# Kernel optimization log

Measured on AMD Instinct MI355X. Metric: run time of the kernel, lower is better.

The kernel has to match this reference:

```python
import jax, jax.numpy as jnp
import numpy as np

N_NODES = 10000
N_EDGES = 160000
N_FEAT = 512
HEADS = 8
HID = 128
OUT = 16


def setup_inputs() -> dict:
    key = jax.random.key(0)
    ks = jax.random.split(key, 16)
    inp = {
        'node_features': jax.random.normal(ks[0], (N_NODES, N_FEAT), jnp.float32),
        'edge_src': jax.random.randint(ks[1], (N_EDGES,), 0, N_NODES, jnp.int32),
        'edge_dst': jax.random.randint(ks[2], (N_EDGES,), 0, N_NODES, jnp.int32),
        # GAT layer params (scaled randn for numerical sanity)
        'W1': jax.random.normal(ks[3], (HEADS, HID, N_FEAT), jnp.float32) * 0.05,
        'a1': jax.random.normal(ks[4], (HEADS, 2 * HID), jnp.float32) * 0.05,
        'W2': jax.random.normal(ks[5], (HEADS, HID, HID), jnp.float32) * 0.05,
        'a2': jax.random.normal(ks[6], (HEADS, 2 * HID), jnp.float32) * 0.05,
        # MLP: LayerNorm(128) -> Linear(128,64) -> LeakyReLU -> Linear(64,16) -> LeakyReLU -> Linear(16,OUT) -> ReLU
        'ln_g': jnp.ones((HID,), jnp.float32),
        'ln_b': jnp.zeros((HID,), jnp.float32),
        'Wl1': jax.random.normal(ks[7], (64, HID), jnp.float32) * 0.05,
        'bl1': jnp.zeros((64,), jnp.float32),
        'Wl2': jax.random.normal(ks[8], (16, 64), jnp.float32) * 0.05,
        'bl2': jnp.zeros((16,), jnp.float32),
        'Wl3': jax.random.normal(ks[9], (OUT, 16), jnp.float32) * 0.05,
        'bl3': jnp.zeros((OUT,), jnp.float32),
    }
    return inp


def gat_layer(x, src, dst, W, a, n_nodes):
    # per-node, per-head projection: h[n,h,d]
    h = jnp.einsum('hdf,nf->nhd', W, x)
    # split attention vector: e_ij = a[:HID].h_i + a[HID:].h_j
    s_i = jnp.einsum('nhd,hd->nh', h, a[:, :HID])  # score contribution of target i
    s_j = jnp.einsum('nhd,hd->nh', h, a[:, HID:])  # score contribution of neighbor j
    e = jax.nn.leaky_relu(s_i[dst] + s_j[src])     # [E,H], negative_slope=0.01 (torch default)
    # segment softmax over edges grouped by dst
    m = jax.ops.segment_max(e, dst, num_segments=n_nodes)           # [N,H]
    m = jnp.where(jnp.isfinite(m), m, 0.0)
    ex = jnp.exp(e - m[dst])                                        # [E,H]
    denom = jax.ops.segment_sum(ex, dst, num_segments=n_nodes)      # [N,H]
    alpha = ex / jnp.where(denom > 0, denom, 1.0)[dst]              # [E,H]
    # scatter-accumulate weighted neighbor embeddings
    agg = jax.ops.segment_sum(alpha[:, :, None] * h[src], dst, num_segments=n_nodes)  # [N,H,HID]
    # average over heads, ELU (matches 1/attn_heads * attn_sum -> ELU)
    return jax.nn.elu(agg.mean(axis=1))  # [N,HID]


def reference(node_features, edge_src, edge_dst, W1, a1, W2, a2,
              ln_g, ln_b, Wl1, bl1, Wl2, bl2, Wl3, bl3):
    n = node_features.shape[0]
    emb1 = gat_layer(node_features, edge_src, edge_dst, W1, a1, n)
    emb2 = gat_layer(emb1, edge_src, edge_dst, W2, a2, n)
    g = emb2.mean(axis=0)  # [HID] graph embedding
    # MLP head (dropout = identity at inference)
    mu = g.mean()
    var = ((g - mu) ** 2).mean()
    gn = (g - mu) / jnp.sqrt(var + 1e-5) * ln_g + ln_b
    x = jax.nn.leaky_relu(Wl1 @ gn + bl1)
    x = jax.nn.leaky_relu(Wl2 @ x + bl2)
    return jax.nn.relu(Wl3 @ x + bl3)
```

## Files before the change

### kernel.cpp

```cpp
#include <hip/hip_runtime.h>
#include <math.h>

#define N_NODES 10000
#define N_EDGES 160000
#define N_FEAT  512
#define HEADS   8
#define HID     128

typedef __attribute__((ext_vector_type(8))) short bf16x8;
typedef __attribute__((ext_vector_type(4))) float f32x4;
typedef __attribute__((ext_vector_type(2))) float v2f;

__device__ inline unsigned short f2bf_rne(float f) {
  unsigned int u = __float_as_uint(f);
  unsigned int r = u + 0x7fffu + ((u >> 16) & 1u);
  return (unsigned short)(r >> 16);
}
__device__ inline float bf2f(unsigned int b) {
  return __uint_as_float(b << 16);
}

__device__ inline void split_body(const float* __restrict__ in,
                                  unsigned short* __restrict__ hi,
                                  unsigned short* __restrict__ lo,
                                  int R, int K8, int idx) {
  int r = idx & 15;
  int t = idx >> 4;
  int kq = t % K8;
  int rb = t / K8;
  int row = rb * 16 + r;
  float v[8] = {0.f, 0.f, 0.f, 0.f, 0.f, 0.f, 0.f, 0.f};
  if (row < R) {
    const float* p = in + (size_t)row * (K8 * 8) + kq * 8;
    float4 a = *(const float4*)p;
    float4 b = *(const float4*)(p + 4);
    v[0] = a.x; v[1] = a.y; v[2] = a.z; v[3] = a.w;
    v[4] = b.x; v[5] = b.y; v[6] = b.z; v[7] = b.w;
  }
  union { unsigned short u[8]; int4 v4; } H, L;
  #pragma unroll
  for (int e = 0; e < 8; ++e) {
    unsigned short hb_ = f2bf_rne(v[e]);
    H.u[e] = hb_;
    L.u[e] = f2bf_rne(v[e] - bf2f(hb_));
  }
  *(int4*)&hi[(size_t)idx * 8] = H.v4;
  if (lo) *(int4*)&lo[(size_t)idx * 8] = L.v4;
}

__global__ __launch_bounds__(256)
void split_frag2(const float* __restrict__ in1, unsigned short* __restrict__ hi1,
                 int R1, int K81, int total1, int nb1,
                 const float* __restrict__ in2, unsigned short* __restrict__ hi2,
                 int R2, int K82, int total2, int nb2,
                 const int* __restrict__ edst, int* __restrict__ deg, int E,
                 const float* __restrict__ av1, const float* __restrict__ W2p,
                 const float* __restrict__ av2,
                 float* __restrict__ wt1, float* __restrict__ wt2) {
  int b = (int)blockIdx.x;
  int tid = threadIdx.x;
  if (b < nb1) {
    int idx = b * 256 + tid;
    if (idx < total1) split_body(in1, hi1, nullptr, R1, K81, idx);
  } else if (b < nb1 + nb2) {
    int idx = (b - nb1) * 256 + tid;
    if (idx < total2) split_body(in2, hi2, nullptr, R2, K82, idx);
  } else {
    int nbE = (E + 255) / 256;
    int eb = b - nb1 - nb2;
    if (eb < nbE) {
      int e = eb * 256 + tid;
      if (e < E) atomicAdd(&deg[edst[e]], 1);
    } else {
      int wb = eb - nbE;
      if (wb < 32) {
        int o = wb * 256 + tid;
        int f = o & 511, ii = (o >> 9) & 1, h = o >> 10;
        const float* Wp = in2 + (size_t)h * HID * N_FEAT + f;
        const float* ap = av1 + h * 2 * HID + ii * HID;
        float c0 = 0.f, c1 = 0.f;
        for (int d = 0; d < HID; d += 2) {
          c0 = fmaf(Wp[(size_t)d * N_FEAT], ap[d], c0);
          c1 = fmaf(Wp[(size_t)(d + 1) * N_FEAT], ap[d + 1], c1);
        }
        wt1[o] = c0 + c1;
      } else {
        int o = (wb - 32) * 256 + tid;
        int f = o & 127, ii = (o >> 7) & 1, h = o >> 8;
        const float* Wp = W2p + (size_t)h * HID * HID + f;
        const float* ap = av2 + h * 2 * HID + ii * HID;
        float c0 = 0.f, c1 = 0.f;
        for (int d = 0; d < HID; d += 2) {
          c0 = fmaf(Wp[(size_t)d * HID], ap[d], c0);
          c1 = fmaf(Wp[(size_t)(d + 1) * HID], ap[d + 1], c1);
        }
        wt2[o] = c0 + c1;
      }
    }
  }
}

__global__ __launch_bounds__(256, 3)
void gemm_frag(const unsigned short* __restrict__ Afh,
               const unsigned short* __restrict__ Bfh,
               unsigned short* __restrict__ hb,
               int M, int K) {
  int tid = threadIdx.x;
  int wave = tid >> 6, lane = tid & 63;
  int r = lane & 15, q = lane >> 4;
  int wr = wave >> 1, wc = wave & 1;

  int blk = blockIdx.x;
  int mtile = blk % 80;
  int head = blk / 80;
  int m0 = mtile * 128;
  int K8 = K >> 3;

  const bf16x8* pA = (const bf16x8*)Afh;
  const bf16x8* pB = (const bf16x8*)Bfh;
  size_t rstep = (size_t)K8 * 16;
  size_t aidx = (size_t)((m0 >> 4) + wr * 4) * rstep + (size_t)q * 16 + r;
  size_t bidx = (size_t)(head * 8 + wc * 4) * rstep + (size_t)q * 16 + r;

  f32x4 acc[4][4] = {};

  for (int k0 = 0; k0 < K; k0 += 64, aidx += 128, bidx += 128) {
    bf16x8 a[8], b[8];
    #pragma unroll
    for (int i = 0; i < 4; ++i) {
      a[i]     = pA[aidx + i * rstep];
      b[i]     = pB[bidx + i * rstep];
      a[i + 4] = pA[aidx + i * rstep + 64];
      b[i + 4] = pB[bidx + i * rstep + 64];
    }
    #pragma unroll
    for (int i = 0; i < 4; ++i)
      #pragma unroll
      for (int j = 0; j < 4; ++j)
        acc[i][j] = __builtin_amdgcn_mfma_f32_16x16x32_bf16(a[i], b[j], acc[i][j], 0, 0, 0);
    #pragma unroll
    for (int i = 0; i < 4; ++i)
      #pragma unroll
      for (int j = 0; j < 4; ++j)
        acc[i][j] = __builtin_amdgcn_mfma_f32_16x16x32_bf16(a[i + 4], b[j + 4], acc[i][j], 0, 0, 0);
  }

  #pragma unroll
  for (int i = 0; i < 4; ++i)
    #pragma unroll
    for (int reg = 0; reg < 4; ++reg) {
      int row = m0 + wr * 64 + i * 16 + q * 4 + reg;
      if (row < M) {
        #pragma unroll
        for (int j = 0; j < 4; ++j)
          hb[((size_t)head * M + row) * HID + wc * 64 + j * 16 + r] =
              f2bf_rne(acc[i][j][reg]);
      }
    }
}

__global__ __launch_bounds__(1024)
void scan_score(const int* __restrict__ deg, int* __restrict__ off, int N,
                const float* __restrict__ x, const float* __restrict__ wt1,
                float* __restrict__ si, float* __restrict__ sj) {
  if (blockIdx.x == 0) {
    __shared__ int sums[1024];
    const int PER = 10;
    int tid = threadIdx.x;
    int base = tid * PER;
    int loc[PER];
    int run = 0;
    #pragma unroll
    for (int j = 0; j < PER; ++j) {
      int v = (base + j < N) ? deg[base + j] : 0;
      run += v;
      loc[j] = run;
    }
    sums[tid] = run;
    __syncthreads();
    for (int o = 1; o < 1024; o <<= 1) {
      int v = (tid >= o) ? sums[tid - o] : 0;
      __syncthreads();
      sums[tid] += v;
      __syncthreads();
    }
    int ex = sums[tid] - run;
    if (tid == 0) off[0] = 0;
    #pragma unroll
    for (int j = 0; j < PER; ++j)
      if (base + j < N) off[base + j + 1] = ex + loc[j];
    return;
  }
  __shared__ float wl[8192];
  int tid = threadIdx.x;
  #pragma unroll
  for (int k = 0; k < 8; ++k) wl[tid + k * 1024] = wt1[tid + k * 1024];
  __syncthreads();
  int wv = tid >> 6, lane = tid & 63;
  int rr = lane >> 4, sl = lane & 15;
  int n = ((int)blockIdx.x - 1) * 64 + wv * 4 + rr;
  if (n >= N) return;
  const float* xp = x + (size_t)n * N_FEAT + sl * 4;
  float acc[16];
  #pragma unroll
  for (int t = 0; t < 16; ++t) acc[t] = 0.f;
  #pragma unroll
  for (int k = 0; k < 8; ++k) {
    float4 xv = *(const float4*)(xp + k * 64);
    #pragma unroll
    for (int t = 0; t < 16; ++t) {
      float4 w4 = *(const float4*)&wl[t * 512 + k * 64 + sl * 4];
      acc[t] = fmaf(xv.x, w4.x, fmaf(xv.y, w4.y, fmaf(xv.z, w4.z, fmaf(xv.w, w4.w, acc[t]))));
    }
  }
  #pragma unroll
  for (int o = 1; o <= 8; o <<= 1)
    #pragma unroll
    for (int t = 0; t < 16; ++t) acc[t] += __shfl_xor(acc[t], o);
  float out = acc[0];
  #pragma unroll
  for (int t = 1; t < 16; ++t) out = (sl == t) ? acc[t] : out;
  int h = sl >> 1;
  if (sl & 1) sj[(size_t)h * N + n] = out;
  else        si[(size_t)h * N + n] = out;
}

__global__ void fill_kernel(const int* __restrict__ src, const int* __restrict__ dst,
                            const int* __restrict__ off, int* __restrict__ cursor,
                            int* __restrict__ ssrc, int E) {
  int e = blockIdx.x * blockDim.x + threadIdx.x;
  if (e < E) {
    int d = dst[e];
    int p = atomicAdd(&cursor[d], 1);
    ssrc[off[d] + p] = src[e];
  }
}

__global__ __launch_bounds__(512)
void gat_aggregate8(const unsigned short* __restrict__ hb,
                    const float* __restrict__ si, const float* __restrict__ sj,
                    const int* __restrict__ off, const int* __restrict__ ssrc,
                    unsigned short* __restrict__ aggb, int N) {
  __shared__ int2 prs[8][4][32];
  int head = blockIdx.x & 7;
  int wv = threadIdx.x >> 6;
  int lane = threadIdx.x & 63;
  int grp = lane >> 4;
  int sl = lane & 15;
  int n = (blockIdx.x >> 3) * 32 + wv * 4 + grp;
  const unsigned short* hbase = hb + (size_t)head * N * HID;
  const float* sjh = sj + (size_t)head * N;
  bool nv = n < N;
  int begin = 0, deg = 0;
  float s_i = 0.f;
  if (nv) {
    begin = off[n];
    deg = off[n + 1] - begin;
    s_i = si[(size_t)head * N + n];
  }

  int src0 = 0, src1 = 0;
  float sc0 = -INFINITY, sc1 = -INFINITY;
  if (sl < deg) {
    src0 = ssrc[begin + sl];
    float t = s_i + sjh[src0];
    sc0 = t > 0.f ? t : 0.01f * t;
  }
  if (16 + sl < deg) {
    src1 = ssrc[begin + 16 + sl];
    float t = s_i + sjh[src1];
    sc1 = t > 0.f ? t : 0.01f * t;
  }
  float m = fmaxf(sc0, sc1);
  for (int e2 = 32 + sl; e2 < deg; e2 += 16) {
    int s = ssrc[begin + e2];
    float t = s_i + sjh[s];
    t = t > 0.f ? t : 0.01f * t;
    m = fmaxf(m, t);
  }
  #pragma unroll
  for (int o = 1; o <= 8; o <<= 1) m = fmaxf(m, __shfl_xor(m, o));

  float w0 = (sl < deg) ? __expf(sc0 - m) : 0.f;
  float w1 = (16 + sl < deg) ? __expf(sc1 - m) : 0.f;
  float den = w0 + w1;
  for (int e2 = 32 + sl; e2 < deg; e2 += 16) {
    int s = ssrc[begin + e2];
    float t = s_i + sjh[s];
    t = t > 0.f ? t : 0.01f * t;
    den += __expf(t - m);
  }
  #pragma unroll
  for (int o = 1; o <= 8; o <<= 1) den += __shfl_xor(den, o);

  prs[wv][grp][sl] = make_int2(src0, __float_as_int(w0));
  prs[wv][grp][16 + sl] = make_int2(src1, __float_as_int(w1));
  __asm__ volatile("s_waitcnt lgkmcnt(0)" ::: "memory");

  v2f a01 = {0.f, 0.f}, a23 = {0.f, 0.f}, a45 = {0.f, 0.f}, a67 = {0.f, 0.f};
  int dmin = deg < 32 ? deg : 32;
  for (int e0 = 0; e0 < dmin; e0 += 4) {
    int2 p[4];
    #pragma unroll
    for (int u = 0; u < 4; ++u) p[u] = prs[wv][grp][e0 + u];
    int4 pv[4];
    #pragma unroll
    for (int u = 0; u < 4; ++u)
      pv[u] = *(const int4*)&hbase[(size_t)p[u].x * HID + sl * 8];
    #pragma unroll
    for (int u = 0; u < 4; ++u) {
      float w = __int_as_float(p[u].y);
      v2f w2 = {w, w};
      int4 q = pv[u];
      v2f t0 = {bf2f((unsigned)q.x & 0xffffu), __uint_as_float((unsigned)q.x & 0xffff0000u)};
      v2f t1 = {bf2f((unsigned)q.y & 0xffffu), __uint_as_float((unsigned)q.y & 0xffff0000u)};
      v2f t2 = {bf2f((unsigned)q.z & 0xffffu), __uint_as_float((unsigned)q.z & 0xffff0000u)};
      v2f t3 = {bf2f((unsigned)q.w & 0xffffu), __uint_as_float((unsigned)q.w & 0xffff0000u)};
      a01 += w2 * t0;
      a23 += w2 * t1;
      a45 += w2 * t2;
      a67 += w2 * t3;
    }
  }
  for (int e2 = 32; e2 < deg; ++e2) {
    int s = ssrc[begin + e2];
    float t = s_i + sjh[s];
    t = t > 0.f ? t : 0.01f * t;
    float w = __expf(t - m);
    v2f w2 = {w, w};
    int4 q = *(const int4*)&hbase[(size_t)s * HID + sl * 8];
    v2f t0 = {bf2f((unsigned)q.x & 0xffffu), __uint_as_float((unsigned)q.x & 0xffff0000u)};
    v2f t1 = {bf2f((unsigned)q.y & 0xffffu), __uint_as_float((unsigned)q.y & 0xffff0000u)};
    v2f t2 = {bf2f((unsigned)q.z & 0xffffu), __uint_as_float((unsigned)q.z & 0xffff0000u)};
    v2f t3 = {bf2f((unsigned)q.w & 0xffffu), __uint_as_float((unsigned)q.w & 0xffff0000u)};
    a01 += w2 * t0; a23 += w2 * t1; a45 += w2 * t2; a67 += w2 * t3;
  }

  if (nv) {
    float inv = den > 0.f ? 1.0f / den : 0.f;
    union { unsigned short u[8]; int4 v4; } P;
    P.u[0] = f2bf_rne(a01.x * inv); P.u[1] = f2bf_rne(a01.y * inv);
    P.u[2] = f2bf_rne(a23.x * inv); P.u[3] = f2bf_rne(a23.y * inv);
    P.u[4] = f2bf_rne(a45.x * inv); P.u[5] = f2bf_rne(a45.y * inv);
    P.u[6] = f2bf_rne(a67.x * inv); P.u[7] = f2bf_rne(a67.y * inv);
    *(int4*)&aggb[((size_t)head * N + n) * HID + sl * 8] = P.v4;
  }
}

__global__ __launch_bounds__(256)
void headmean_frag_w2(const unsigned short* __restrict__ aggb,
                      unsigned short* __restrict__ hiA,
                      int N, int nbHM,
                      const float* __restrict__ W2, unsigned short* __restrict__ hiB,
                      int totalB,
                      const float* __restrict__ wt2,
                      float* __restrict__ si, float* __restrict__ sj) {
  if ((int)blockIdx.x >= nbHM) {
    int idx = (blockIdx.x - nbHM) * 256 + threadIdx.x;
    if (idx < totalB) split_body(W2, hiB, nullptr, HEADS * HID, 16, idx);
    return;
  }
  __shared__ float wl[2048];
  __shared__ float sred[16][16][17];
  int tid = threadIdx.x;
  #pragma unroll
  for (int k = 0; k < 8; ++k) wl[tid + k * 256] = wt2[tid + k * 256];
  __syncthreads();
  int idx = blockIdx.x * 256 + tid;
  int r = idx & 15;
  int kq = (idx >> 4) & 15;
  int rb = idx >> 8;
  int n = rb * 16 + r;
  float s[8] = {0.f, 0.f, 0.f, 0.f, 0.f, 0.f, 0.f, 0.f};
  if (n < N) {
    #pragma unroll
    for (int hh = 0; hh < HEADS; ++hh) {
      int4 pv = *(const int4*)&aggb[((size_t)hh * N + n) * HID + kq * 8];
      s[0] += bf2f((unsigned)pv.x & 0xffffu);
      s[1] += __uint_as_float((unsigned)pv.x & 0xffff0000u);
      s[2] += bf2f((unsigned)pv.y & 0xffffu);
      s[3] += __uint_as_float((unsigned)pv.y & 0xffff0000u);
      s[4] += bf2f((unsigned)pv.z & 0xffffu);
      s[5] += __uint_as_float((unsigned)pv.z & 0xffff0000u);
      s[6] += bf2f((unsigned)pv.w & 0xffffu);
      s[7] += __uint_as_float((unsigned)pv.w & 0xffff0000u);
    }
  }
  float p[16];
  #pragma unroll
  for (int t = 0; t < 16; ++t) p[t] = 0.f;
  union { unsigned short u[8]; int4 v4; } H;
  #pragma unroll
  for (int e = 0; e < 8; ++e) {
    float v = s[e] * (1.0f / HEADS);
    v = v > 0.f ? v : (__expf(v) - 1.0f);
    #pragma unroll
    for (int t = 0; t < 16; ++t) p[t] = fmaf(v, wl[t * 128 + kq * 8 + e], p[t]);
    H.u[e] = f2bf_rne(v);
  }
  *(int4*)&hiA[(size_t)idx * 8] = H.v4;
  #pragma unroll
  for (int t = 0; t < 16; ++t) sred[kq][r][t] = p[t];
  __syncthreads();
  {
    int rr = tid >> 4, t = tid & 15;
    float sum = 0.f;
    #pragma unroll
    for (int k = 0; k < 16; ++k) sum += sred[k][rr][t];
    int nn = rb * 16 + rr;
    if (nn < N) {
      int h = t >> 1;
      if (t & 1) sj[(size_t)h * N + nn] = sum;
      else       si[(size_t)h * N + nn] = sum;
    }
  }
}

__global__ __launch_bounds__(256)
void headmean_pool(const unsigned short* __restrict__ aggb, float* __restrict__ g,
                   int N) {
  __shared__ float sm[16][128];
  int t = threadIdx.x;
  int nl = t >> 4, dg = t & 15;
  int n = blockIdx.x * 16 + nl;
  float v[8] = {0.f, 0.f, 0.f, 0.f, 0.f, 0.f, 0.f, 0.f};
  if (n < N) {
    #pragma unroll
    for (int hh = 0; hh < HEADS; ++hh) {
      int4 pv = *(const int4*)&aggb[((size_t)hh * N + n) * HID + dg * 8];
      v[0] += bf2f((unsigned)pv.x & 0xffffu);
      v[1] += __uint_as_float((unsigned)pv.x & 0xffff0000u);
      v[2] += bf2f((unsigned)pv.y & 0xffffu);
      v[3] += __uint_as_float((unsigned)pv.y & 0xffff0000u);
      v[4] += bf2f((unsigned)pv.z & 0xffffu);
      v[5] += __uint_as_float((unsigned)pv.z & 0xffff0000u);
      v[6] += bf2f((unsigned)pv.w & 0xffffu);
      v[7] += __uint_as_float((unsigned)pv.w & 0xffff0000u);
    }
    #pragma unroll
    for (int e = 0; e < 8; ++e) {
      float x = v[e] * (1.0f / HEADS);
      v[e] = x > 0.f ? x : (__expf(x) - 1.0f);
    }
  }
  #pragma unroll
  for (int e = 0; e < 8; ++e) sm[nl][dg * 8 + e] = v[e];
  __syncthreads();
  if (t < 128) {
    float s = 0.f;
    #pragma unroll
    for (int nn = 0; nn < 16; ++nn) s += sm[nn][t];
    atomicAdd(&g[t], s);
  }
}

__global__ __launch_bounds__(128)
void mlp_kernel(const float* __restrict__ g, const float* __restrict__ ln_g,
                const float* __restrict__ ln_b, const float* __restrict__ Wl1,
                const float* __restrict__ bl1, const float* __restrict__ Wl2,
                const float* __restrict__ bl2, const float* __restrict__ Wl3,
                const float* __restrict__ bl3, float* __restrict__ out, float invN) {
  __shared__ float red[128];
  __shared__ float gn[128];
  __shared__ float x1[64];
  __shared__ float x2[16];
  int t = threadIdx.x;
  float gg = g[t] * invN;
  red[t] = gg;
  __syncthreads();
  for (int o = 64; o > 0; o >>= 1) {
    if (t < o) red[t] += red[t + o];
    __syncthreads();
  }
  float mu = red[0] * (1.0f / HID);
  __syncthreads();
  float dv = gg - mu;
  red[t] = dv * dv;
  __syncthreads();
  for (int o = 64; o > 0; o >>= 1) {
    if (t < o) red[t] += red[t + o];
    __syncthreads();
  }
  float var = red[0] * (1.0f / HID);
  gn[t] = dv / sqrtf(var + 1e-5f) * ln_g[t] + ln_b[t];
  __syncthreads();
  if (t < 64) {
    float s = bl1[t];
    for (int k = 0; k < 128; ++k) s += Wl1[t * 128 + k] * gn[k];
    x1[t] = s > 0.f ? s : 0.01f * s;
  }
  __syncthreads();
  if (t < 16) {
    float s = bl2[t];
    for (int k = 0; k < 64; ++k) s += Wl2[t * 64 + k] * x1[k];
    x2[t] = s > 0.f ? s : 0.01f * s;
  }
  __syncthreads();
  if (t < 16) {
    float s = bl3[t];
    for (int k = 0; k < 16; ++k) s += Wl3[t * 16 + k] * x2[k];
    out[t] = s > 0.f ? s : 0.f;
  }
}

extern "C" void kernel_launch(void* const* d_in, const int* in_sizes, int n_in,
                              void* d_out, int out_size, void* d_ws, size_t ws_size,
                              hipStream_t stream) {
  const float* x    = (const float*)d_in[0];
  const int*   esrc = (const int*)d_in[1];
  const int*   edst = (const int*)d_in[2];
  const float* W1   = (const float*)d_in[3];
  const float* a1   = (const float*)d_in[4];
  const float* W2   = (const float*)d_in[5];
  const float* a2   = (const float*)d_in[6];
  const float* ln_g = (const float*)d_in[7];
  const float* ln_b = (const float*)d_in[8];
  const float* Wl1  = (const float*)d_in[9];
  const float* bl1  = (const float*)d_in[10];
  const float* Wl2  = (const float*)d_in[11];
  const float* bl2  = (const float*)d_in[12];
  const float* Wl3  = (const float*)d_in[13];
  const float* bl3  = (const float*)d_in[14];
  float* out = (float*)d_out;

  const int RBPAD = 640;

  unsigned short* aggb = (unsigned short*)d_ws;
  float* si   = (float*)(aggb + (size_t)N_NODES * HEADS * HID);
  float* sj   = si + N_NODES * HEADS;
  float* g    = sj + N_NODES * HEADS;
  int*   deg  = (int*)(g + 128);
  int*   cur  = deg + N_NODES;
  int*   off  = cur + N_NODES;
  int*   ssrc = off + 10004;
  unsigned short* Afh = (unsigned short*)(ssrc + N_EDGES);
  float* wt1 = (float*)(Afh + (size_t)RBPAD * 64 * 128);
  float* wt2 = wt1 + 8192;
  unsigned short* Bfh = (unsigned short*)(wt1 + (size_t)RBPAD * 64 * 64);
  unsigned short* hb  = Bfh + (size_t)2 * 64 * 64 * 128;

  hipMemsetAsync(g, 0, 128 * sizeof(float) + 2 * N_NODES * sizeof(int), stream);

  int gemmGrid = 80 * HEADS;
  int aggGrid = ((N_NODES + 31) / 32) * 8;

  {
    int totalA = RBPAD * 64 * 16;
    int nbA = (totalA + 255) / 256;
    int totalB = 64 * 64 * 16;
    int nbB = (totalB + 255) / 256;
    int nbE = (N_EDGES + 255) / 256;
    int nbW = 40;
    split_frag2<<<nbA + nbB + nbE + nbW, 256, 0, stream>>>(
        x, Afh, N_NODES, 64, totalA, nbA,
        W1, Bfh, HEADS * HID, 64, totalB, nbB,
        edst, deg, N_EDGES,
        a1, W2, a2, wt1, wt2);
  }
  scan_score<<<1 + (N_NODES + 63) / 64, 1024, 0, stream>>>(deg, off, N_NODES,
                                                           x, wt1, si, sj);
  fill_kernel<<<(N_EDGES + 255) / 256, 256, 0, stream>>>(esrc, edst, off, cur, ssrc, N_EDGES);

  gemm_frag<<<gemmGrid, 256, 0, stream>>>(Afh, Bfh, hb, N_NODES, N_FEAT);
  gat_aggregate8<<<aggGrid, 512, 0, stream>>>(hb, si, sj, off, ssrc, aggb, N_NODES);
  {
    int nbHM = (N_NODES + 15) / 16;
    int totalB = 64 * 16 * 16;
    int nbB = (totalB + 255) / 256;
    headmean_frag_w2<<<nbHM + nbB, 256, 0, stream>>>(aggb, Afh, N_NODES, nbHM,
                                                     W2, Bfh, totalB,
                                                     wt2, si, sj);
  }

  gemm_frag<<<gemmGrid, 256, 0, stream>>>(Afh, Bfh, hb, N_NODES, HID);
  gat_aggregate8<<<aggGrid, 512, 0, stream>>>(hb, si, sj, off, ssrc, aggb, N_NODES);

  headmean_pool<<<(N_NODES + 15) / 16, 256, 0, stream>>>(aggb, g, N_NODES);
  mlp_kernel<<<1, 128, 0, stream>>>(g, ln_g, ln_b, Wl1, bl1, Wl2, bl2, Wl3, bl3,
                                    out, 1.0f / N_NODES);
}
```

Before: 251.7 us.

## Replace CSR build with fixed-slot adjacency and fuse score into GEMM launch

Replaces the degree count, prefix-scan and fill passes with a single pass that atomically places each edge's source into a fixed 32-slot bucket per destination, spilling extras to a global overflow list. This removes two kernel launches and their serialization. The layer-1 score computation is merged into the GEMM launch as extra blocks, and the W2 bf16 conversion moves into the first kernel. The aggregation loop is unrolled to 8 edges. Nodes with more than 32 in-edges now scan the whole overflow list, which is costly if such nodes are common. The order of edges within a node now depends on atomics, so floating-point summation order is nondeterministic.

```diff
diff --git a/kernel.cpp b/kernel.cpp
--- a/kernel.cpp
+++ b/kernel.cpp
@@ -22,7 +22,6 @@
 
 __device__ inline void split_body(const float* __restrict__ in,
                                   unsigned short* __restrict__ hi,
-                                  unsigned short* __restrict__ lo,
                                   int R, int K8, int idx) {
   int r = idx & 15;
   int t = idx >> 4;
@@ -37,15 +36,10 @@
     v[0] = a.x; v[1] = a.y; v[2] = a.z; v[3] = a.w;
     v[4] = b.x; v[5] = b.y; v[6] = b.z; v[7] = b.w;
   }
-  union { unsigned short u[8]; int4 v4; } H, L;
-  #pragma unroll
-  for (int e = 0; e < 8; ++e) {
-    unsigned short hb_ = f2bf_rne(v[e]);
-    H.u[e] = hb_;
-    L.u[e] = f2bf_rne(v[e] - bf2f(hb_));
-  }
+  union { unsigned short u[8]; int4 v4; } H;
+  #pragma unroll
+  for (int e = 0; e < 8; ++e) H.u[e] = f2bf_rne(v[e]);
   *(int4*)&hi[(size_t)idx * 8] = H.v4;
-  if (lo) *(int4*)&lo[(size_t)idx * 8] = L.v4;
 }
 
 __global__ __launch_bounds__(256)
@@ -53,24 +47,39 @@
                  int R1, int K81, int total1, int nb1,
                  const float* __restrict__ in2, unsigned short* __restrict__ hi2,
                  int R2, int K82, int total2, int nb2,
-                 const int* __restrict__ edst, int* __restrict__ deg, int E,
-                 const float* __restrict__ av1, const float* __restrict__ W2p,
-                 const float* __restrict__ av2,
+                 const float* __restrict__ W2p, unsigned short* __restrict__ hi3,
+                 int total3, int nb3,
+                 const int* __restrict__ esrc, const int* __restrict__ edst,
+                 int* __restrict__ deg, int* __restrict__ slots,
+                 int2* __restrict__ ovf, int* __restrict__ cnt, int E,
+                 const float* __restrict__ av1, const float* __restrict__ av2,
                  float* __restrict__ wt1, float* __restrict__ wt2) {
   int b = (int)blockIdx.x;
   int tid = threadIdx.x;
   if (b < nb1) {
     int idx = b * 256 + tid;
-    if (idx < total1) split_body(in1, hi1, nullptr, R1, K81, idx);
+    if (idx < total1) split_body(in1, hi1, R1, K81, idx);
   } else if (b < nb1 + nb2) {
     int idx = (b - nb1) * 256 + tid;
-    if (idx < total2) split_body(in2, hi2, nullptr, R2, K82, idx);
+    if (idx < total2) split_body(in2, hi2, R2, K82, idx);
+  } else if (b < nb1 + nb2 + nb3) {
+    int idx = (b - nb1 - nb2) * 256 + tid;
+    if (idx < total3) split_body(W2p, hi3, HEADS * HID, 16, idx);
   } else {
     int nbE = (E + 255) / 256;
-    int eb = b - nb1 - nb2;
+    int eb = b - nb1 - nb2 - nb3;
     if (eb < nbE) {
       int e = eb * 256 + tid;
-      if (e < E) atomicAdd(&deg[edst[e]], 1);
+      if (e < E) {
+        int d = edst[e], s = esrc[e];
+        int p = atomicAdd(&deg[d], 1);
+        if (p < 32) {
+          slots[d * 32 + p] = s;
+        } else {
+          int q = atomicAdd(&cnt[1], 1);
+          if (q < E) ovf[q] = make_int2(d, s);
+        }
+      }
     } else {
       int wb = eb - nbE;
       if (wb < 32) {
@@ -101,11 +110,48 @@
 }
 
 __global__ __launch_bounds__(256, 3)
-void gemm_frag(const unsigned short* __restrict__ Afh,
-               const unsigned short* __restrict__ Bfh,
-               unsigned short* __restrict__ hb,
-               int M, int K) {
+void gemm_score(const unsigned short* __restrict__ Afh,
+                const unsigned short* __restrict__ Bfh,
+                unsigned short* __restrict__ hb,
+                int M, int K, int nbGemm,
+                const float* __restrict__ x, const float* __restrict__ wt1,
+                float* __restrict__ si, float* __restrict__ sj, int N) {
   int tid = threadIdx.x;
+  if ((int)blockIdx.x >= nbGemm) {
+    __shared__ float wl[8192];
+    #pragma unroll
+    for (int k = 0; k < 32; ++k) wl[tid + k * 256] = wt1[tid + k * 256];
+    __syncthreads();
+    int wv = tid >> 6, lane = tid & 63;
+    int rr = lane >> 4, sl = lane & 15;
+    int n = ((int)blockIdx.x - nbGemm) * 16 + wv * 4 + rr;
+    if (n >= N) return;
+    const float* xp = x + (size_t)n * N_FEAT + sl * 4;
+    float acc[16];
+    #pragma unroll
+    for (int t = 0; t < 16; ++t) acc[t] = 0.f;
+    #pragma unroll
+    for (int k = 0; k < 8; ++k) {
+      float4 xv = *(const float4*)(xp + k * 64);
+      #pragma unroll
+      for (int t = 0; t < 16; ++t) {
+        float4 w4 = *(const float4*)&wl[t * 512 + k * 64 + sl * 4];
+        acc[t] = fmaf(xv.x, w4.x, fmaf(xv.y, w4.y, fmaf(xv.z, w4.z, fmaf(xv.w, w4.w, acc[t]))));
+      }
+    }
+    #pragma unroll
+    for (int o = 1; o <= 8; o <<= 1)
+      #pragma unroll
+      for (int t = 0; t < 16; ++t) acc[t] += __shfl_xor(acc[t], o);
+    float outv = acc[0];
+    #pragma unroll
+    for (int t = 1; t < 16; ++t) outv = (sl == t) ? acc[t] : outv;
+    int h = sl >> 1;
+    if (sl & 1) sj[(size_t)h * N + n] = outv;
+    else        si[(size_t)h * N + n] = outv;
+    return;
+  }
+
   int wave = tid >> 6, lane = tid & 63;
   int r = lane & 15, q = lane >> 4;
   int wr = wave >> 1, wc = wave & 1;
@@ -159,87 +205,11 @@
     }
 }
 
-__global__ __launch_bounds__(1024)
-void scan_score(const int* __restrict__ deg, int* __restrict__ off, int N,
-                const float* __restrict__ x, const float* __restrict__ wt1,
-                float* __restrict__ si, float* __restrict__ sj) {
-  if (blockIdx.x == 0) {
-    __shared__ int sums[1024];
-    const int PER = 10;
-    int tid = threadIdx.x;
-    int base = tid * PER;
-    int loc[PER];
-    int run = 0;
-    #pragma unroll
-    for (int j = 0; j < PER; ++j) {
-      int v = (base + j < N) ? deg[base + j] : 0;
-      run += v;
-      loc[j] = run;
-    }
-    sums[tid] = run;
-    __syncthreads();
-    for (int o = 1; o < 1024; o <<= 1) {
-      int v = (tid >= o) ? sums[tid - o] : 0;
-      __syncthreads();
-      sums[tid] += v;
-      __syncthreads();
-    }
-    int ex = sums[tid] - run;
-    if (tid == 0) off[0] = 0;
-    #pragma unroll
-    for (int j = 0; j < PER; ++j)
-      if (base + j < N) off[base + j + 1] = ex + loc[j];
-    return;
-  }
-  __shared__ float wl[8192];
-  int tid = threadIdx.x;
-  #pragma unroll
-  for (int k = 0; k < 8; ++k) wl[tid + k * 1024] = wt1[tid + k * 1024];
-  __syncthreads();
-  int wv = tid >> 6, lane = tid & 63;
-  int rr = lane >> 4, sl = lane & 15;
-  int n = ((int)blockIdx.x - 1) * 64 + wv * 4 + rr;
-  if (n >= N) return;
-  const float* xp = x + (size_t)n * N_FEAT + sl * 4;
-  float acc[16];
-  #pragma unroll
-  for (int t = 0; t < 16; ++t) acc[t] = 0.f;
-  #pragma unroll
-  for (int k = 0; k < 8; ++k) {
-    float4 xv = *(const float4*)(xp + k * 64);
-    #pragma unroll
-    for (int t = 0; t < 16; ++t) {
-      float4 w4 = *(const float4*)&wl[t * 512 + k * 64 + sl * 4];
-      acc[t] = fmaf(xv.x, w4.x, fmaf(xv.y, w4.y, fmaf(xv.z, w4.z, fmaf(xv.w, w4.w, acc[t]))));
-    }
-  }
-  #pragma unroll
-  for (int o = 1; o <= 8; o <<= 1)
-    #pragma unroll
-    for (int t = 0; t < 16; ++t) acc[t] += __shfl_xor(acc[t], o);
-  float out = acc[0];
-  #pragma unroll
-  for (int t = 1; t < 16; ++t) out = (sl == t) ? acc[t] : out;
-  int h = sl >> 1;
-  if (sl & 1) sj[(size_t)h * N + n] = out;
-  else        si[(size_t)h * N + n] = out;
-}
-
-__global__ void fill_kernel(const int* __restrict__ src, const int* __restrict__ dst,
-                            const int* __restrict__ off, int* __restrict__ cursor,
-                            int* __restrict__ ssrc, int E) {
-  int e = blockIdx.x * blockDim.x + threadIdx.x;
-  if (e < E) {
-    int d = dst[e];
-    int p = atomicAdd(&cursor[d], 1);
-    ssrc[off[d] + p] = src[e];
-  }
-}
-
 __global__ __launch_bounds__(512)
-void gat_aggregate8(const unsigned short* __restrict__ hb,
+void gat_aggregate9(const unsigned short* __restrict__ hb,
                     const float* __restrict__ si, const float* __restrict__ sj,
-                    const int* __restrict__ off, const int* __restrict__ ssrc,
+                    const int* __restrict__ deg, const int* __restrict__ slots,
+                    const int2* __restrict__ ovf, const int* __restrict__ cnt,
                     unsigned short* __restrict__ aggb, int N) {
   __shared__ int2 prs[8][4][32];
   int head = blockIdx.x & 7;
@@ -251,44 +221,55 @@
   const unsigned short* hbase = hb + (size_t)head * N * HID;
   const float* sjh = sj + (size_t)head * N;
   bool nv = n < N;
-  int begin = 0, deg = 0;
+  int dg = 0;
   float s_i = 0.f;
   if (nv) {
-    begin = off[n];
-    deg = off[n + 1] - begin;
+    dg = deg[n];
     s_i = si[(size_t)head * N + n];
   }
+  int sbase = n * 32;
 
   int src0 = 0, src1 = 0;
   float sc0 = -INFINITY, sc1 = -INFINITY;
-  if (sl < deg) {
-    src0 = ssrc[begin + sl];
+  if (sl < dg) {
+    src0 = slots[sbase + sl];
     float t = s_i + sjh[src0];
     sc0 = t > 0.f ? t : 0.01f * t;
   }
-  if (16 + sl < deg) {
-    src1 = ssrc[begin + 16 + sl];
+  if (16 + sl < dg) {
+    src1 = slots[sbase + 16 + sl];
     float t = s_i + sjh[src1];
     sc1 = t > 0.f ? t : 0.01f * t;
   }
   float m = fmaxf(sc0, sc1);
-  for (int e2 = 32 + sl; e2 < deg; e2 += 16) {
-    int s = ssrc[begin + e2];
-    float t = s_i + sjh[s];
-    t = t > 0.f ? t : 0.01f * t;
-    m = fmaxf(m, t);
+  int oc = 0;
+  if (dg > 32) {
+    oc = cnt[1];
+    if (oc > N_EDGES) oc = N_EDGES;
+    for (int e2 = sl; e2 < oc; e2 += 16) {
+      int2 pe = ovf[e2];
+      if (pe.x == n) {
+        float t = s_i + sjh[pe.y];
+        t = t > 0.f ? t : 0.01f * t;
+        m = fmaxf(m, t);
+      }
+    }
   }
   #pragma unroll
   for (int o = 1; o <= 8; o <<= 1) m = fmaxf(m, __shfl_xor(m, o));
 
-  float w0 = (sl < deg) ? __expf(sc0 - m) : 0.f;
-  float w1 = (16 + sl < deg) ? __expf(sc1 - m) : 0.f;
+  float w0 = (sl < dg) ? __expf(sc0 - m) : 0.f;
+  float w1 = (16 + sl < dg) ? __expf(sc1 - m) : 0.f;
   float den = w0 + w1;
-  for (int e2 = 32 + sl; e2 < deg; e2 += 16) {
-    int s = ssrc[begin + e2];
-    float t = s_i + sjh[s];
-    t = t > 0.f ? t : 0.01f * t;
-    den += __expf(t - m);
+  if (dg > 32) {
+    for (int e2 = sl; e2 < oc; e2 += 16) {
+      int2 pe = ovf[e2];
+      if (pe.x == n) {
+        float t = s_i + sjh[pe.y];
+        t = t > 0.f ? t : 0.01f * t;
+        den += __expf(t - m);
+      }
+    }
   }
   #pragma unroll
   for (int o = 1; o <= 8; o <<= 1) den += __shfl_xor(den, o);
@@ -298,17 +279,17 @@
   __asm__ volatile("s_waitcnt lgkmcnt(0)" ::: "memory");
 
   v2f a01 = {0.f, 0.f}, a23 = {0.f, 0.f}, a45 = {0.f, 0.f}, a67 = {0.f, 0.f};
-  int dmin = deg < 32 ? deg : 32;
-  for (int e0 = 0; e0 < dmin; e0 += 4) {
-    int2 p[4];
-    #pragma unroll
-    for (int u = 0; u < 4; ++u) p[u] = prs[wv][grp][e0 + u];
-    int4 pv[4];
-    #pragma unroll
-    for (int u = 0; u < 4; ++u)
+  int dmin = dg < 32 ? dg : 32;
+  for (int e0 = 0; e0 < dmin; e0 += 8) {
+    int2 p[8];
+    #pragma unroll
+    for (int u = 0; u < 8; ++u) p[u] = prs[wv][grp][e0 + u];
+    int4 pv[8];
+    #pragma unroll
+    for (int u = 0; u < 8; ++u)
       pv[u] = *(const int4*)&hbase[(size_t)p[u].x * HID + sl * 8];
     #pragma unroll
-    for (int u = 0; u < 4; ++u) {
+    for (int u = 0; u < 8; ++u) {
       float w = __int_as_float(p[u].y);
       v2f w2 = {w, w};
       int4 q = pv[u];
@@ -322,18 +303,21 @@
       a67 += w2 * t3;
     }
   }
-  for (int e2 = 32; e2 < deg; ++e2) {
-    int s = ssrc[begin + e2];
-    float t = s_i + sjh[s];
-    t = t > 0.f ? t : 0.01f * t;
-    float w = __expf(t - m);
-    v2f w2 = {w, w};
-    int4 q = *(const int4*)&hbase[(size_t)s * HID + sl * 8];
-    v2f t0 = {bf2f((unsigned)q.x & 0xffffu), __uint_as_float((unsigned)q.x & 0xffff0000u)};
-    v2f t1 = {bf2f((unsigned)q.y & 0xffffu), __uint_as_float((unsigned)q.y & 0xffff0000u)};
-    v2f t2 = {bf2f((unsigned)q.z & 0xffffu), __uint_as_float((unsigned)q.z & 0xffff0000u)};
-    v2f t3 = {bf2f((unsigned)q.w & 0xffffu), __uint_as_float((unsigned)q.w & 0xffff0000u)};
-    a01 += w2 * t0; a23 += w2 * t1; a45 += w2 * t2; a67 += w2 * t3;
+  if (dg > 32) {
+    for (int e2 = 0; e2 < oc; ++e2) {
+      int2 pe = ovf[e2];
+      if (pe.x != n) continue;
+      float t = s_i + sjh[pe.y];
+      t = t > 0.f ? t : 0.01f * t;
+      float w = __expf(t - m);
+      v2f w2 = {w, w};
+      int4 q = *(const int4*)&hbase[(size_t)pe.y * HID + sl * 8];
+      v2f t0 = {bf2f((unsigned)q.x & 0xffffu), __uint_as_float((unsigned)q.x & 0xffff0000u)};
+      v2f t1 = {bf2f((unsigned)q.y & 0xffffu), __uint_as_float((unsigned)q.y & 0xffff0000u)};
+      v2f t2 = {bf2f((unsigned)q.z & 0xffffu), __uint_as_float((unsigned)q.z & 0xffff0000u)};
+      v2f t3 = {bf2f((unsigned)q.w & 0xffffu), __uint_as_float((unsigned)q.w & 0xffff0000u)};
+      a01 += w2 * t0; a23 += w2 * t1; a45 += w2 * t2; a67 += w2 * t3;
+    }
   }
 
   if (nv) {
@@ -348,18 +332,10 @@
 }
 
 __global__ __launch_bounds__(256)
-void headmean_frag_w2(const unsigned short* __restrict__ aggb,
-                      unsigned short* __restrict__ hiA,
-                      int N, int nbHM,
-                      const float* __restrict__ W2, unsigned short* __restrict__ hiB,
-                      int totalB,
-                      const float* __restrict__ wt2,
-                      float* __restrict__ si, float* __restrict__ sj) {
-  if ((int)blockIdx.x >= nbHM) {
-    int idx = (blockIdx.x - nbHM) * 256 + threadIdx.x;
-    if (idx < totalB) split_body(W2, hiB, nullptr, HEADS * HID, 16, idx);
-    return;
-  }
+void headmean_frag2(const unsigned short* __restrict__ aggb,
+                    unsigned short* __restrict__ hiA, int N,
+                    const float* __restrict__ wt2,
+                    float* __restrict__ si, float* __restrict__ sj) {
   __shared__ float wl[2048];
   __shared__ float sred[16][16][17];
   int tid = threadIdx.x;
@@ -530,18 +506,20 @@
   float* sj   = si + N_NODES * HEADS;
   float* g    = sj + N_NODES * HEADS;
   int*   deg  = (int*)(g + 128);
-  int*   cur  = deg + N_NODES;
-  int*   off  = cur + N_NODES;
-  int*   ssrc = off + 10004;
-  unsigned short* Afh = (unsigned short*)(ssrc + N_EDGES);
-  float* wt1 = (float*)(Afh + (size_t)RBPAD * 64 * 128);
-  float* wt2 = wt1 + 8192;
-  unsigned short* Bfh = (unsigned short*)(wt1 + (size_t)RBPAD * 64 * 64);
-  unsigned short* hb  = Bfh + (size_t)2 * 64 * 64 * 128;
-
-  hipMemsetAsync(g, 0, 128 * sizeof(float) + 2 * N_NODES * sizeof(int), stream);
+  int*   cnt  = deg + N_NODES;
+  int*   slots= cnt + 4;
+  int2*  ovf  = (int2*)(slots + (size_t)N_NODES * 32);
+  float* wt1  = (float*)(ovf + N_EDGES);
+  float* wt2  = wt1 + 8192;
+  unsigned short* Afh  = (unsigned short*)(wt2 + 2048);
+  unsigned short* Bfh  = Afh + (size_t)RBPAD * 64 * 128;
+  unsigned short* Bfh2 = Bfh + (size_t)1024 * 512;
+  unsigned short* hb   = Bfh2 + (size_t)1024 * 128;
+
+  hipMemsetAsync(g, 0, 128 * sizeof(float) + (N_NODES + 4) * sizeof(int), stream);
 
   int gemmGrid = 80 * HEADS;
+  int scoreGrid = (N_NODES + 15) / 16;
   int aggGrid = ((N_NODES + 31) / 32) * 8;
 
   {
@@ -549,31 +527,29 @@
     int nbA = (totalA + 255) / 256;
     int totalB = 64 * 64 * 16;
     int nbB = (totalB + 255) / 256;
+    int totalB2 = 64 * 16 * 16;
+    int nbB2 = (totalB2 + 255) / 256;
     int nbE = (N_EDGES + 255) / 256;
     int nbW = 40;
-    split_frag2<<<nbA + nbB + nbE + nbW, 256, 0, stream>>>(
+    split_frag2<<<nbA + nbB + nbB2 + nbE + nbW, 256, 0, stream>>>(
         x, Afh, N_NODES, 64, totalA, nbA,
         W1, Bfh, HEADS * HID, 64, totalB, nbB,
-        edst, deg, N_EDGES,
-        a1, W2, a2, wt1, wt2);
-  }
-  scan_score<<<1 + (N_NODES + 63) / 64, 1024, 0, stream>>>(deg, off, N_NODES,
-                                                           x, wt1, si, sj);
-  fill_kernel<<<(N_EDGES + 255) / 256, 256, 0, stream>>>(esrc, edst, off, cur, ssrc, N_EDGES);
-
-  gemm_frag<<<gemmGrid, 256, 0, stream>>>(Afh, Bfh, hb, N_NODES, N_FEAT);
-  gat_aggregate8<<<aggGrid, 512, 0, stream>>>(hb, si, sj, off, ssrc, aggb, N_NODES);
-  {
-    int nbHM = (N_NODES + 15) / 16;
-    int totalB = 64 * 16 * 16;
-    int nbB = (totalB + 255) / 256;
-    headmean_frag_w2<<<nbHM + nbB, 256, 0, stream>>>(aggb, Afh, N_NODES, nbHM,
-                                                     W2, Bfh, totalB,
-                                                     wt2, si, sj);
-  }
-
-  gemm_frag<<<gemmGrid, 256, 0, stream>>>(Afh, Bfh, hb, N_NODES, HID);
-  gat_aggregate8<<<aggGrid, 512, 0, stream>>>(hb, si, sj, off, ssrc, aggb, N_NODES);
+        W2, Bfh2, totalB2, nbB2,
+        esrc, edst, deg, slots, ovf, cnt, N_EDGES,
+        a1, a2, wt1, wt2);
+  }
+
+  gemm_score<<<gemmGrid + scoreGrid, 256, 0, stream>>>(
+      Afh, Bfh, hb, N_NODES, N_FEAT, gemmGrid, x, wt1, si, sj, N_NODES);
+  gat_aggregate9<<<aggGrid, 512, 0, stream>>>(hb, si, sj, deg, slots, ovf, cnt,
+                                              aggb, N_NODES);
+  headmean_frag2<<<(N_NODES + 15) / 16, 256, 0, stream>>>(aggb, Afh, N_NODES,
+                                                          wt2, si, sj);
+
+  gemm_score<<<gemmGrid, 256, 0, stream>>>(
+      Afh, Bfh2, hb, N_NODES, HID, gemmGrid, nullptr, nullptr, nullptr, nullptr, 0);
+  gat_aggregate9<<<aggGrid, 512, 0, stream>>>(hb, si, sj, deg, slots, ovf, cnt,
+                                              aggb, N_NODES);
 
   headmean_pool<<<(N_NODES + 15) / 16, 256, 0, stream>>>(aggb, g, N_NODES);
   mlp_kernel<<<1, 128, 0, stream>>>(g, ln_g, ln_b, Wl1, bl1, Wl2, bl2, Wl3, bl3,
```

New measurement: 242.1 us. 1.04x faster.
